# Kernel optimization log

Measured on AMD Instinct MI355X. Metric: run time of the kernel, lower is better.

Reference implementation:

```python
import math
import jax, jax.numpy as jnp
import numpy as np

B, C, NH, H, W = 8, 512, 4, 64, 64
CH = C // 8          # qkv channels = 64
HC = CH // NH        # head channels = 16


def _pos_encoding(c, h, w):
    # Faithful to torch code, including the raw memory reinterpretation of
    # pos_h (h, c) -> (1, c, h, 1) and pos_w (c//2, 2w) -> (1, c, 1, w).
    ph = jnp.arange(h, dtype=jnp.float32)[:, None]            # (h, 1)
    pw = jnp.arange(w, dtype=jnp.float32)[None, :]            # (1, w)
    div = jnp.exp(jnp.arange(0, c, 2, dtype=jnp.float32) * (-(math.log(10000.0) / c)))
    pos_h = ph * div[None, :]                                  # (h, c/2)
    pos_w = pw * div[:, None]                                  # (c/2, w)
    pos_h = jnp.concatenate([jnp.sin(pos_h), jnp.cos(pos_h)], axis=1)  # (h, c)
    pos_w = jnp.concatenate([jnp.sin(pos_w), jnp.cos(pos_w)], axis=1)  # (c/2, 2w)
    pos_h = pos_h.reshape(1, c, h, 1)   # raw view, as in torch
    pos_w = pos_w.reshape(1, c, 1, w)   # raw view, as in torch
    return pos_h + pos_w                # (1, c, h, w)


def _conv1x1(x, w, b):
    return jnp.einsum('bchw,oc->bohw', x, w) + b[None, :, None, None]


def setup_inputs() -> dict:
    key = jax.random.key(0)
    ks = jax.random.split(key, 6)
    s = 0.02
    return {
        'x':  jax.random.normal(ks[0], (B, C, H, W), dtype=jnp.float32),
        'wq': jax.random.normal(ks[1], (CH, C), dtype=jnp.float32) * s,
        'bq': jnp.zeros((CH,), dtype=jnp.float32),
        'wk': jax.random.normal(ks[2], (CH, C), dtype=jnp.float32) * s,
        'bk': jnp.zeros((CH,), dtype=jnp.float32),
        'wv': jax.random.normal(ks[3], (CH, C), dtype=jnp.float32) * s,
        'bv': jnp.zeros((CH,), dtype=jnp.float32),
        'wo': jax.random.normal(ks[4], (C, CH), dtype=jnp.float32) * s,
        'bo': jnp.zeros((C,), dtype=jnp.float32),
        'gamma': jnp.full((1,), 0.5, dtype=jnp.float32),  # nonzero to exercise whole graph
    }


def reference(x, wq, bq, wk, bk, wv, bv, wo, bo, gamma):
    b, c, h, w = x.shape
    nh, hc = NH, HC
    x = x + _pos_encoding(c, h, w)

    q = _conv1x1(x, wq, bq).reshape(b, nh, hc, h, w)
    k = _conv1x1(x, wk, bk).reshape(b, nh, hc, h, w)
    v = _conv1x1(x, wv, bv).reshape(b, nh, hc, h, w)

    # column (H) and row (W) views
    q_H = q.transpose(0, 1, 4, 2, 3).reshape(b * nh * w, hc, h).transpose(0, 2, 1)  # (bnw, h, hc)
    q_W = q.transpose(0, 1, 3, 2, 4).reshape(b * nh * h, hc, w).transpose(0, 2, 1)  # (bnh, w, hc)
    k_H = k.transpose(0, 1, 4, 2, 3).reshape(b * nh * w, hc, h)
    k_W = k.transpose(0, 1, 3, 2, 4).reshape(b * nh * h, hc, w)
    v_H = v.transpose(0, 1, 4, 2, 3).reshape(b * nh * w, hc, h)
    v_W = v.transpose(0, 1, 3, 2, 4).reshape(b * nh * h, hc, w)

    inf_mask = jnp.where(jnp.eye(h, dtype=bool), -jnp.inf, 0.0).astype(x.dtype)  # (h, h)
    energy_H = (jnp.matmul(q_H, k_H) + inf_mask[None]).reshape(b, nh, w, h, h).transpose(0, 2, 1, 3, 4)  # (b,w,nh,h,h)
    energy_W = jnp.matmul(q_W, k_W).reshape(b, nh, h, w, w).transpose(0, 2, 1, 3, 4)                     # (b,h,nh,w,w)

    conc = jax.nn.softmax(jnp.concatenate([energy_H, energy_W], axis=4), axis=4)  # (b,w,nh,h,h+w)

    att_H = conc[..., :h].transpose(0, 2, 1, 3, 4).reshape(b * nh * w, h, h)
    # NOTE: faithful to torch: (b,h,nh,w,w) is flattened in (b,h,nh) order
    att_W = conc[..., h:h + w].reshape(b * nh * h, w, w)

    out_H = jnp.matmul(v_H, att_H.transpose(0, 2, 1))
    out_H = out_H.reshape(b, nh, w, hc, h).transpose(0, 3, 4, 1, 2).reshape(b, nh * hc, h, w)
    out_W = jnp.matmul(v_W, att_W.transpose(0, 2, 1))
    out_W = out_W.reshape(b, nh, h, hc, w).transpose(0, 3, 1, 4, 2).reshape(b, nh * hc, h, w)

    out = _conv1x1(out_H + out_W, wo, bo)
    return gamma * out + x
```

## Files before the change

kernel.cpp:

```cpp
#include <hip/hip_runtime.h>
#include <math.h>


typedef unsigned int u32;
typedef unsigned short u16;
typedef __attribute__((ext_vector_type(8))) short short8;
typedef __attribute__((ext_vector_type(4))) float f32x4;

__device__ __forceinline__ u16 f2bf(float v) {
    u32 u = __float_as_uint(v);
    u32 r = (u + 0x7FFFu + ((u >> 16) & 1u)) >> 16;
    return (u16)r;
}

__device__ __forceinline__ void gll16(const void* g, void* l) {
    __builtin_amdgcn_global_load_lds(
        (const __attribute__((address_space(1))) u32*)g,
        (__attribute__((address_space(3))) u32*)l, 16, 0, 0);
}

__global__ __launch_bounds__(64) void pos_kernel(float* __restrict__ PH,
                                                 float* __restrict__ PW) {
    const float r = 0.03597789207798663f;
    int c = blockIdx.x;
    int t = threadIdx.x;
    int i = c >> 3;
    int j = ((c & 7) << 6) | t;
    float ph;
    if (j < 256) ph = sinf((float)i * expf(-(float)j * r));
    else         ph = cosf((float)i * expf(-(float)(j - 256) * r));
    PH[c * 64 + t] = ph;
    int tt = c >> 1;
    float dv = expf(-(float)tt * r);
    PW[c * 64 + t] = (c & 1) ? cosf((float)t * dv) : sinf((float)t * dv);
}

__global__ __launch_bounds__(256) void wconv_kernel(
    const float* __restrict__ wq, const float* __restrict__ wk,
    const float* __restrict__ wv, const float* __restrict__ wo,
    u16* __restrict__ WT, u16* __restrict__ WOb) {
    int i = blockIdx.x * 256 + threadIdx.x;
    if (i < 98304) {
        float v;
        if (i < 32768)      v = wq[i];
        else if (i < 65536) v = wk[i - 32768];
        else                v = wv[i - 65536];
        WT[i] = f2bf(v);
    } else {
        WOb[i - 98304] = f2bf(wo[i - 98304]);
    }
}

__global__ __launch_bounds__(256) void xpose_kernel(
    const float* __restrict__ x, const float* __restrict__ PH,
    const float* __restrict__ PW, u16* __restrict__ XT) {
    __shared__ u16 T[64 * 68];
    int ct = blockIdx.x;
    int pt = blockIdx.y;
    int b  = blockIdx.z;
    int tid = threadIdx.x;
    int c0 = ct * 64;
    const size_t xb = ((size_t)b * 512 + c0) * 4096 + pt * 64;
#pragma unroll
    for (int it = 0; it < 16; ++it) {
        int idx = tid + it * 256;
        int cl = idx >> 6, pl = idx & 63;
        float v = x[xb + (size_t)cl * 4096 + pl]
                + PH[(c0 + cl) * 64 + pt] + PW[(c0 + cl) * 64 + pl];
        T[pl * 68 + cl] = f2bf(v);
    }
    __syncthreads();
#pragma unroll
    for (int jt = 0; jt < 4; ++jt) {
        int row = jt * 16 + (tid >> 4);
        int cq  = tid & 15;
        ushort4 val = *(const ushort4*)&T[row * 68 + cq * 4];
        *(ushort4*)&XT[((size_t)b * 4096 + pt * 64 + row) * 512 + c0 + cq * 4] = val;
    }
}

__global__ __launch_bounds__(256) void qkvm_kernel(
    const u16* __restrict__ XT, const u16* __restrict__ WT,
    const float* __restrict__ bq, const float* __restrict__ bk,
    const float* __restrict__ bv,
    u16* __restrict__ QHt, u16* __restrict__ QWt,
    u16* __restrict__ KHt, u16* __restrict__ KWt,
    u16* __restrict__ VHt, u16* __restrict__ Vb) {
    __shared__ u16 Ab[64 * 64];
    __shared__ u16 Bb[128 * 64];
    int pt = blockIdx.x;
    int mg = blockIdx.y;
    int b  = blockIdx.z;
    int tid  = threadIdx.x;
    int w    = tid >> 6;
    int lane = tid & 63;
    int ln15 = lane & 15, quad = lane >> 4;
    int p0 = pt * 128;
    const u16* Wg = WT + mg * 64 * 512;
    const u16* Xg = XT + ((size_t)b * 4096 + p0) * 512;

    f32x4 acc[4][2];
#pragma unroll
    for (int mf = 0; mf < 4; ++mf)
#pragma unroll
        for (int pf = 0; pf < 2; ++pf)
            acc[mf][pf] = (f32x4){0.f, 0.f, 0.f, 0.f};

    for (int kc = 0; kc < 512; kc += 64) {
        __syncthreads();
#pragma unroll
        for (int it = 0; it < 2; ++it) {
            int idx = tid + it * 256;
            int r = idx >> 3, s = idx & 7;
            gll16(Wg + r * 512 + kc + ((s ^ (r & 7)) * 8), &Ab[idx * 8]);
        }
#pragma unroll
        for (int it = 0; it < 4; ++it) {
            int idx = tid + it * 256;
            int r = idx >> 3, s = idx & 7;
            gll16(Xg + (size_t)r * 512 + kc + ((s ^ (r & 7)) * 8), &Bb[idx * 8]);
        }
        __syncthreads();
#pragma unroll
        for (int ks = 0; ks < 2; ++ks) {
            int cs = ks * 4 + quad;
            short8 af[4], bf[2];
#pragma unroll
            for (int mf = 0; mf < 4; ++mf) {
                int row = mf * 16 + ln15;
                af[mf] = *(const short8*)&Ab[row * 64 + ((cs ^ (row & 7)) * 8)];
            }
#pragma unroll
            for (int pf = 0; pf < 2; ++pf) {
                int row = w * 32 + pf * 16 + ln15;
                bf[pf] = *(const short8*)&Bb[row * 64 + ((cs ^ (row & 7)) * 8)];
            }
#pragma unroll
            for (int mf = 0; mf < 4; ++mf)
#pragma unroll
                for (int pf = 0; pf < 2; ++pf)
                    acc[mf][pf] = __builtin_amdgcn_mfma_f32_16x16x32_bf16(
                        af[mf], bf[pf], acc[mf][pf], 0, 0, 0);
        }
    }

    const float* bias = (mg == 0) ? bq : (mg == 1) ? bk : bv;
    if (mg == 2) {
#pragma unroll
        for (int mf = 0; mf < 4; ++mf)
#pragma unroll
            for (int pf = 0; pf < 2; ++pf) {
                int p = p0 + w * 32 + pf * 16 + ln15;
                int h = p >> 6, wc = p & 63;
#pragma unroll
                for (int reg = 0; reg < 4; ++reg) {
                    int hc = quad * 4 + reg;
                    int m  = mf * 16 + hc;
                    u16 bfv = f2bf(acc[mf][pf][reg] + bias[m]);
                    VHt[(((b * 4 + mf) * 64 + wc) * 16 + hc) * 64 + h] = bfv;
                    Vb[((size_t)(b * 64 + m)) * 4096 + p] = bfv;
                }
            }
    } else {
        u16* Ht = (mg == 1) ? KHt : QHt;
        u16* Wt = (mg == 1) ? KWt : QWt;
#pragma unroll
        for (int mf = 0; mf < 4; ++mf)
#pragma unroll
            for (int pf = 0; pf < 2; ++pf) {
                int p = p0 + w * 32 + pf * 16 + ln15;
                int h = p >> 6, wc = p & 63;
                ushort4 pk;
                pk.x = f2bf(acc[mf][pf][0] + bias[mf * 16 + quad * 4 + 0]);
                pk.y = f2bf(acc[mf][pf][1] + bias[mf * 16 + quad * 4 + 1]);
                pk.z = f2bf(acc[mf][pf][2] + bias[mf * 16 + quad * 4 + 2]);
                pk.w = f2bf(acc[mf][pf][3] + bias[mf * 16 + quad * 4 + 3]);
                *(ushort4*)&Ht[(((b * 4 + mf) * 64 + wc) * 64 + h) * 16 + quad * 4] = pk;
                *(ushort4*)&Wt[(((b * 4 + mf) * 64 + h) * 64 + wc) * 16 + quad * 4] = pk;
            }
    }
}

__global__ __launch_bounds__(256, 4) void attn_kernel(
    const u16* __restrict__ QHt, const u16* __restrict__ QWt,
    const u16* __restrict__ KHt, const u16* __restrict__ KWt,
    const u16* __restrict__ VHt, const u16* __restrict__ Vb,
    float* __restrict__ OH, float* __restrict__ OW) {
    __shared__ u16 A_lds[64 * 40];
    __shared__ u16 B_lds[128 * 40];
    __shared__ u16 VH_lds[16 * 72];
    __shared__ u16 VW_lds[16 * 72];
    __shared__ u16 P_lds[64 * 144];

    int a = blockIdx.x, n = blockIdx.y, b = blockIdx.z;
    int tid  = threadIdx.x;
    int w    = tid >> 6;
    int lane = tid & 63;
    int ln15 = lane & 15, quad = lane >> 4;
    int nv = a >> 4;
    int hv = ((a & 15) << 2) | n;

    const int cb = ((b * 4 + n) * 64 + a) << 10;
    const u16* vb = Vb + ((size_t)(b * 64 + nv * 16)) * 4096 + hv * 64;

    {
        int t = tid & 127;
        const short8 z8 = {0, 0, 0, 0, 0, 0, 0, 0};
        if (tid < 128) {
            short8 vA = *(const short8*)(QHt + cb + t * 8);
            *(short8*)&A_lds[(t >> 1) * 40 + (t & 1) * 8] = vA;
            short8 vK = *(const short8*)(KHt + cb + t * 8);
            *(short8*)&B_lds[(t >> 1) * 40 + (t & 1) * 8] = vK;
            *(short8*)&B_lds[(t >> 1) * 40 + 16 + (t & 1) * 8] = z8;
            short8 vV = *(const short8*)(VHt + cb + t * 8);
            *(short8*)&VH_lds[(t >> 3) * 72 + (t & 7) * 8] = vV;
        } else {
            short8 vA = *(const short8*)(QWt + cb + t * 8);
            *(short8*)&A_lds[(t >> 1) * 40 + 16 + (t & 1) * 8] = vA;
            short8 vK = *(const short8*)(KWt + cb + t * 8);
            *(short8*)&B_lds[(64 + (t >> 1)) * 40 + 16 + (t & 1) * 8] = vK;
            *(short8*)&B_lds[(64 + (t >> 1)) * 40 + (t & 1) * 8] = z8;
            short8 vV = *(const short8*)(vb + (t >> 3) * 4096 + (t & 7) * 8);
            *(short8*)&VW_lds[(t >> 3) * 72 + (t & 7) * 8] = vV;
        }
    }
    __syncthreads();

    const f32x4 zf = {0.f, 0.f, 0.f, 0.f};
    short8 af = *(const short8*)&A_lds[(w * 16 + ln15) * 40 + quad * 8];
    f32x4 acc[8];
#pragma unroll
    for (int nt = 0; nt < 8; ++nt) {
        short8 bf = *(const short8*)&B_lds[(nt * 16 + ln15) * 40 + quad * 8];
        acc[nt] = __builtin_amdgcn_mfma_f32_16x16x32_bf16(af, bf, zf, 0, 0, 0);
    }

#pragma unroll
    for (int nt = 0; nt < 4; ++nt)
#pragma unroll
        for (int r = 0; r < 4; ++r)
            if (nt * 16 + ln15 == w * 16 + quad * 4 + r) acc[nt][r] = -1e30f;

    float inv[4];
#pragma unroll
    for (int r = 0; r < 4; ++r) {
        float mrow = acc[0][r];
#pragma unroll
        for (int nt = 1; nt < 8; ++nt) mrow = fmaxf(mrow, acc[nt][r]);
        mrow = fmaxf(mrow, __shfl_xor(mrow, 1, 64));
        mrow = fmaxf(mrow, __shfl_xor(mrow, 2, 64));
        mrow = fmaxf(mrow, __shfl_xor(mrow, 4, 64));
        mrow = fmaxf(mrow, __shfl_xor(mrow, 8, 64));
        float s = 0.f;
#pragma unroll
        for (int nt = 0; nt < 8; ++nt) {
            float e = __expf(acc[nt][r] - mrow);
            acc[nt][r] = e;
            s += e;
        }
        s += __shfl_xor(s, 1, 64);
        s += __shfl_xor(s, 2, 64);
        s += __shfl_xor(s, 4, 64);
        s += __shfl_xor(s, 8, 64);
        inv[r] = 1.0f / s;
    }
#pragma unroll
    for (int nt = 0; nt < 8; ++nt)
#pragma unroll
        for (int r = 0; r < 4; ++r)
            P_lds[(w * 16 + quad * 4 + r) * 144 + nt * 16 + ln15] =
                f2bf(acc[nt][r] * inv[r]);
    __syncthreads();

    int prow = (w * 16 + ln15) * 144;
    short8 a0 = *(const short8*)&P_lds[prow +       quad * 8];
    short8 a1 = *(const short8*)&P_lds[prow + 32  + quad * 8];
    short8 a2 = *(const short8*)&P_lds[prow + 64  + quad * 8];
    short8 a3 = *(const short8*)&P_lds[prow + 96  + quad * 8];
    short8 b0 = *(const short8*)&VH_lds[ln15 * 72 +      quad * 8];
    short8 b1 = *(const short8*)&VH_lds[ln15 * 72 + 32 + quad * 8];
    short8 c0 = *(const short8*)&VW_lds[ln15 * 72 +      quad * 8];
    short8 c1 = *(const short8*)&VW_lds[ln15 * 72 + 32 + quad * 8];
    f32x4 oH = __builtin_amdgcn_mfma_f32_16x16x32_bf16(a0, b0, zf, 0, 0, 0);
    oH = __builtin_amdgcn_mfma_f32_16x16x32_bf16(a1, b1, oH, 0, 0, 0);
    f32x4 oW = __builtin_amdgcn_mfma_f32_16x16x32_bf16(a2, c0, zf, 0, 0, 0);
    oW = __builtin_amdgcn_mfma_f32_16x16x32_bf16(a3, c1, oW, 0, 0, 0);

#pragma unroll
    for (int r = 0; r < 4; ++r) {
        int dl = quad * 4 + r;
        OH[((b * 64 + ln15 * 4 + w) * 64 + dl * 4 + n) * 64 + a] = oH[r];
        OW[((b * 64 + ln15 * 4 + nv) * 64 + w * 16 + dl) * 64 + hv] = oW[r];
    }
}

__global__ __launch_bounds__(256) void sconv_kernel(
    const float* __restrict__ OH, const float* __restrict__ OW,
    u16* __restrict__ Sb) {
    __shared__ u16 T[64 * 68];
    int pt = blockIdx.x;
    int b  = blockIdx.y;
    int tid = threadIdx.x;
#pragma unroll
    for (int it = 0; it < 16; ++it) {
        int idx = tid + it * 256;
        int cl = idx >> 6, pl = idx & 63;
        int o = (b * 64 + cl) * 4096 + pt * 64 + pl;
        T[pl * 68 + cl] = f2bf(OH[o] + OW[o]);
    }
    __syncthreads();
#pragma unroll
    for (int jt = 0; jt < 4; ++jt) {
        int row = jt * 16 + (tid >> 4);
        int cq  = tid & 15;
        ushort4 val = *(const ushort4*)&T[row * 68 + cq * 4];
        *(ushort4*)&Sb[((size_t)b * 4096 + pt * 64 + row) * 64 + cq * 4] = val;
    }
}

__global__ __launch_bounds__(256, 4) void finalm_kernel(
    const u16* __restrict__ Sb, const u16* __restrict__ WOb,
    const float* __restrict__ bo, const float* __restrict__ gamma,
    const float* __restrict__ x, const float* __restrict__ PH,
    const float* __restrict__ PW, float* __restrict__ out) {
    __shared__ u16 Ab[64 * 64];
    __shared__ u16 Bb[128 * 64];
    int pt = blockIdx.x;
    int mc = blockIdx.y;
    int b  = blockIdx.z;
    int tid  = threadIdx.x;
    int w    = tid >> 6;
    int lane = tid & 63;
    int ln15 = lane & 15, quad = lane >> 4;
    int p0 = pt * 128, m0 = mc * 64;

    float4 xv[4][2];
#pragma unroll
    for (int mf = 0; mf < 4; ++mf) {
        int m = m0 + mf * 16 + ln15;
#pragma unroll
        for (int pf = 0; pf < 2; ++pf) {
            int pb = p0 + w * 32 + pf * 16 + quad * 4;
            xv[mf][pf] = *(const float4*)&x[((size_t)(b * 512 + m)) * 4096 + pb];
        }
    }

    const u16* Ag = WOb + m0 * 64;
    const u16* Sg = Sb + ((size_t)b * 4096 + p0) * 64;

#pragma unroll
    for (int it = 0; it < 2; ++it) {
        int idx = tid + it * 256;
        int r = idx >> 3, s = idx & 7;
        gll16(Ag + r * 64 + ((s ^ (r & 7)) * 8), &Ab[idx * 8]);
    }
#pragma unroll
    for (int it = 0; it < 4; ++it) {
        int idx = tid + it * 256;
        int r = idx >> 3, s = idx & 7;
        gll16(Sg + r * 64 + ((s ^ (r & 7)) * 8), &Bb[idx * 8]);
    }
    __syncthreads();

    const f32x4 zf = {0.f, 0.f, 0.f, 0.f};
    f32x4 acc[4][2];
#pragma unroll
    for (int mf = 0; mf < 4; ++mf)
#pragma unroll
        for (int pf = 0; pf < 2; ++pf)
            acc[mf][pf] = zf;
#pragma unroll
    for (int ks = 0; ks < 2; ++ks) {
        int cs = ks * 4 + quad;
        short8 af[2], bf[4];
#pragma unroll
        for (int pf = 0; pf < 2; ++pf) {
            int row = w * 32 + pf * 16 + ln15;
            af[pf] = *(const short8*)&Bb[row * 64 + ((cs ^ (row & 7)) * 8)];
        }
#pragma unroll
        for (int mf = 0; mf < 4; ++mf) {
            int row = mf * 16 + ln15;
            bf[mf] = *(const short8*)&Ab[row * 64 + ((cs ^ (row & 7)) * 8)];
        }
#pragma unroll
        for (int mf = 0; mf < 4; ++mf)
#pragma unroll
            for (int pf = 0; pf < 2; ++pf)
                acc[mf][pf] = __builtin_amdgcn_mfma_f32_16x16x32_bf16(
                    af[pf], bf[mf], acc[mf][pf], 0, 0, 0);
    }

    float g = gamma[0];
    int h = pt * 2 + (w >> 1);
    int plb = (w & 1) * 32;
#pragma unroll
    for (int mf = 0; mf < 4; ++mf) {
        int m = m0 + mf * 16 + ln15;
        float bm = bo[m];
        float ph = PH[m * 64 + h];
#pragma unroll
        for (int pf = 0; pf < 2; ++pf) {
            int pb = p0 + w * 32 + pf * 16 + quad * 4;
            size_t o = ((size_t)(b * 512 + m)) * 4096 + pb;
            float4 pwv = *(const float4*)&PW[m * 64 + plb + pf * 16 + quad * 4];
            float4 res;
            res.x = g * (acc[mf][pf][0] + bm) + xv[mf][pf].x + ph + pwv.x;
            res.y = g * (acc[mf][pf][1] + bm) + xv[mf][pf].y + ph + pwv.y;
            res.z = g * (acc[mf][pf][2] + bm) + xv[mf][pf].z + ph + pwv.z;
            res.w = g * (acc[mf][pf][3] + bm) + xv[mf][pf].w + ph + pwv.w;
            *(float4*)&out[o] = res;
        }
    }
}

extern "C" void kernel_launch(void* const* d_in, const int* in_sizes, int n_in,
                              void* d_out, int out_size, void* d_ws, size_t ws_size,
                              hipStream_t stream) {
    const float* x     = (const float*)d_in[0];
    const float* wq    = (const float*)d_in[1];
    const float* bq    = (const float*)d_in[2];
    const float* wk    = (const float*)d_in[3];
    const float* bk    = (const float*)d_in[4];
    const float* wv    = (const float*)d_in[5];
    const float* bv    = (const float*)d_in[6];
    const float* wo    = (const float*)d_in[7];
    const float* bo    = (const float*)d_in[8];
    const float* gamma = (const float*)d_in[9];
    float* out = (float*)d_out;
    float* ws  = (float*)d_ws;

    float* PH = ws;
    float* PW = PH + 32768;
    u16*   WT  = (u16*)(PW + 32768);
    u16*   WOb = WT + 98304;
    u16*   XT  = WOb + 32768;
    u16*   QHt = XT + 16777216;
    u16*   QWt = QHt + 2097152;
    u16*   KHt = QWt + 2097152;
    u16*   KWt = KHt + 2097152;
    u16*   VHt = KWt + 2097152;
    u16*   Vb  = VHt + 2097152;
    float* OH  = (float*)XT;
    float* OW  = OH + 2097152;
    u16*   Sbb = (u16*)(OW + 2097152);

    pos_kernel<<<dim3(512), dim3(64), 0, stream>>>(PH, PW);
    wconv_kernel<<<dim3(512), dim3(256), 0, stream>>>(wq, wk, wv, wo, WT, WOb);
    xpose_kernel<<<dim3(8, 64, 8), dim3(256), 0, stream>>>(x, PH, PW, XT);
    qkvm_kernel<<<dim3(32, 3, 8), dim3(256), 0, stream>>>(
        XT, WT, bq, bk, bv, QHt, QWt, KHt, KWt, VHt, Vb);
    attn_kernel<<<dim3(64, 4, 8), dim3(256), 0, stream>>>(
        QHt, QWt, KHt, KWt, VHt, Vb, OH, OW);
    sconv_kernel<<<dim3(64, 8), dim3(256), 0, stream>>>(OH, OW, Sbb);
    finalm_kernel<<<dim3(32, 8, 8), dim3(256), 0, stream>>>(
        Sbb, WOb, bo, gamma, x, PH, PW, out);
}
```

Before: 231.1 us.

## Stage attention outputs through LDS and store bf16 contiguous blocks

The attention kernel previously wrote fp32 OH/OW with scattered per-element stores. It now converts results to bf16, transposes them through shared memory (reusing P_lds with a wider row pitch), and writes contiguous 1 KB chunks per block. The sum kernel is rewritten to read this blocked bf16 layout with vector loads, which halves the intermediate traffic and coalesces the accesses. In exchange, OH and OW are rounded to bf16 before they are summed, adding one extra rounding step to the output.

Result: faster. 207.7 us (-10.1%).

```diff
diff --git a/kernel.cpp b/kernel.cpp
--- a/kernel.cpp
+++ b/kernel.cpp
@@ -11,6 +11,10 @@
     u32 u = __float_as_uint(v);
     u32 r = (u + 0x7FFFu + ((u >> 16) & 1u)) >> 16;
     return (u16)r;
+}
+
+__device__ __forceinline__ float bf2f(u16 v) {
+    return __uint_as_float(((u32)v) << 16);
 }
 
 __device__ __forceinline__ void gll16(const void* g, void* l) {
@@ -185,12 +189,12 @@
     const u16* __restrict__ QHt, const u16* __restrict__ QWt,
     const u16* __restrict__ KHt, const u16* __restrict__ KWt,
     const u16* __restrict__ VHt, const u16* __restrict__ Vb,
-    float* __restrict__ OH, float* __restrict__ OW) {
+    u16* __restrict__ OHc, u16* __restrict__ OWc) {
     __shared__ u16 A_lds[64 * 40];
     __shared__ u16 B_lds[128 * 40];
     __shared__ u16 VH_lds[16 * 72];
     __shared__ u16 VW_lds[16 * 72];
-    __shared__ u16 P_lds[64 * 144];
+    __shared__ u16 P_lds[64 * 152];
 
     int a = blockIdx.x, n = blockIdx.y, b = blockIdx.z;
     int tid  = threadIdx.x;
@@ -268,11 +272,11 @@
     for (int nt = 0; nt < 8; ++nt)
 #pragma unroll
         for (int r = 0; r < 4; ++r)
-            P_lds[(w * 16 + quad * 4 + r) * 144 + nt * 16 + ln15] =
+            P_lds[(w * 16 + quad * 4 + r) * 152 + nt * 16 + ln15] =
                 f2bf(acc[nt][r] * inv[r]);
     __syncthreads();
 
-    int prow = (w * 16 + ln15) * 144;
+    int prow = (w * 16 + ln15) * 152;
     short8 a0 = *(const short8*)&P_lds[prow +       quad * 8];
     short8 a1 = *(const short8*)&P_lds[prow + 32  + quad * 8];
     short8 a2 = *(const short8*)&P_lds[prow + 64  + quad * 8];
@@ -286,36 +290,56 @@
     f32x4 oW = __builtin_amdgcn_mfma_f32_16x16x32_bf16(a2, c0, zf, 0, 0, 0);
     oW = __builtin_amdgcn_mfma_f32_16x16x32_bf16(a3, c1, oW, 0, 0, 0);
 
+    __syncthreads();
+    u16* eph = P_lds;
+    u16* epw = P_lds + 16 * 68;
 #pragma unroll
     for (int r = 0; r < 4; ++r) {
-        int dl = quad * 4 + r;
-        OH[((b * 64 + ln15 * 4 + w) * 64 + dl * 4 + n) * 64 + a] = oH[r];
-        OW[((b * 64 + ln15 * 4 + nv) * 64 + w * 16 + dl) * 64 + hv] = oW[r];
+        eph[(quad * 4 + r) * 68 + ln15 * 4 + w]   = f2bf(oH[r]);
+        epw[(w * 16 + quad * 4 + r) * 20 + ln15]  = f2bf(oW[r]);
+    }
+    __syncthreads();
+    {
+        int t = tid;
+        ushort4 vh = *(const ushort4*)&eph[(t >> 4) * 68 + (t & 15) * 4];
+        ushort4 vw = *(const ushort4*)&epw[(t >> 2) * 20 + (t & 3) * 4];
+        size_t cbase = (((size_t)b * 4 + n) * 64 + a) * 1024;
+        *(ushort4*)&OHc[cbase + t * 4] = vh;
+        *(ushort4*)&OWc[cbase + t * 4] = vw;
     }
 }
 
 __global__ __launch_bounds__(256) void sconv_kernel(
-    const float* __restrict__ OH, const float* __restrict__ OW,
+    const u16* __restrict__ OHc, const u16* __restrict__ OWc,
     u16* __restrict__ Sb) {
-    __shared__ u16 T[64 * 68];
-    int pt = blockIdx.x;
-    int b  = blockIdx.y;
-    int tid = threadIdx.x;
-#pragma unroll
-    for (int it = 0; it < 16; ++it) {
-        int idx = tid + it * 256;
-        int cl = idx >> 6, pl = idx & 63;
-        int o = (b * 64 + cl) * 4096 + pt * 64 + pl;
-        T[pl * 68 + cl] = f2bf(OH[o] + OW[o]);
-    }
-    __syncthreads();
-#pragma unroll
-    for (int jt = 0; jt < 4; ++jt) {
-        int row = jt * 16 + (tid >> 4);
-        int cq  = tid & 15;
-        ushort4 val = *(const ushort4*)&T[row * 68 + cq * 4];
-        *(ushort4*)&Sb[((size_t)b * 4096 + pt * 64 + row) * 64 + cq * 4] = val;
-    }
+    int h = blockIdx.x;
+    int b = blockIdx.y;
+    int t  = threadIdx.x;
+    int wp = t >> 2;
+    int cq = t & 3;
+
+    const u16* ohp = OHc + ((((size_t)b * 4 + (h & 3)) * 64 + wp) * 1024
+                            + (h >> 2) * 64 + cq * 16);
+    short8 oh0 = *(const short8*)ohp;
+    short8 oh1 = *(const short8*)(ohp + 8);
+
+    const u16* owb = OWc + (((size_t)b * 4 + (wp & 3)) * 64) * 1024 + h * 16 + cq * 4;
+    ushort4 owv[4];
+#pragma unroll
+    for (int nvi = 0; nvi < 4; ++nvi)
+        owv[nvi] = *(const ushort4*)(owb + (size_t)((nvi << 4) | (wp >> 2)) * 1024);
+
+    u16 res[16];
+#pragma unroll
+    for (int j = 0; j < 16; ++j) {
+        u16 ohv = (j < 8) ? (u16)oh0[j] : (u16)oh1[j - 8];
+        const ushort4& q = owv[j & 3];
+        u16 owu = (j >> 2) == 0 ? q.x : (j >> 2) == 1 ? q.y : (j >> 2) == 2 ? q.z : q.w;
+        res[j] = f2bf(bf2f(ohv) + bf2f(owu));
+    }
+    u16* dst = Sb + (((size_t)b * 4096 + h * 64 + wp) * 64 + cq * 16);
+    *(short8*)dst       = *(short8*)&res[0];
+    *(short8*)(dst + 8) = *(short8*)&res[8];
 }
 
 __global__ __launch_bounds__(256, 4) void finalm_kernel(
@@ -441,9 +465,9 @@
     u16*   KWt = KHt + 2097152;
     u16*   VHt = KWt + 2097152;
     u16*   Vb  = VHt + 2097152;
-    float* OH  = (float*)XT;
-    float* OW  = OH + 2097152;
-    u16*   Sbb = (u16*)(OW + 2097152);
+    u16*   OHc = XT;
+    u16*   OWc = OHc + 2097152;
+    u16*   Sbb = OWc + 2097152;
 
     pos_kernel<<<dim3(512), dim3(64), 0, stream>>>(PH, PW);
     wconv_kernel<<<dim3(512), dim3(256), 0, stream>>>(wq, wk, wv, wo, WT, WOb);
@@ -451,8 +475,8 @@
     qkvm_kernel<<<dim3(32, 3, 8), dim3(256), 0, stream>>>(
         XT, WT, bq, bk, bv, QHt, QWt, KHt, KWt, VHt, Vb);
     attn_kernel<<<dim3(64, 4, 8), dim3(256), 0, stream>>>(
-        QHt, QWt, KHt, KWt, VHt, Vb, OH, OW);
-    sconv_kernel<<<dim3(64, 8), dim3(256), 0, stream>>>(OH, OW, Sbb);
+        QHt, QWt, KHt, KWt, VHt, Vb, OHc, OWc);
+    sconv_kernel<<<dim3(64, 8), dim3(256), 0, stream>>>(OHc, OWc, Sbb);
     finalm_kernel<<<dim3(32, 8, 8), dim3(256), 0, stream>>>(
         Sbb, WOb, bo, gamma, x, PH, PW, out);
 }
```
